# Kernel tuning notes

Measured on AMD Instinct MI355X. Metric: run time of the kernel, lower is better.

Reference implementation:

```python
import jax, jax.numpy as jnp
import numpy as np

B, N, C, H = 2, 2048, 1024, 16
D = C // H  # head dim
SCALE = D ** -0.5


def setup_inputs() -> dict:
    key = jax.random.key(0)
    k1, k2, k3 = jax.random.split(key, 3)
    x = jax.random.normal(k1, (B, N, C), dtype=jnp.float32)
    w_qkv = jax.random.normal(k2, (C, 3 * C), dtype=jnp.float32) * (C ** -0.5)
    w_proj = jax.random.normal(k3, (C, C), dtype=jnp.float32) * (C ** -0.5)
    b_proj = jnp.zeros((C,), dtype=jnp.float32)
    return {"x": x, "w_qkv": w_qkv, "w_proj": w_proj, "b_proj": b_proj}


def reference(x, w_qkv, w_proj, b_proj):
    # qkv projection: [B,N,3C] -> [3,B,H,N,D]
    qkv = (x @ w_qkv).reshape(B, N, 3, H, D).transpose(2, 0, 3, 1, 4)
    q, k, v = qkv[0], qkv[1], qkv[2]
    # attention scores [B,H,N,N]
    attn = jnp.einsum("bhnd,bhmd->bhnm", q, k) * SCALE
    attn = jax.nn.softmax(attn, axis=-1)
    # weighted values -> [B,N,C]
    out = jnp.einsum("bhnm,bhmd->bhnd", attn, v)
    out = out.transpose(0, 2, 1, 3).reshape(B, N, C)
    return out @ w_proj + b_proj
```

## Files before the change

kernel.cpp:

```cpp
#include <hip/hip_runtime.h>
#include <hip/hip_bf16.h>

#define BDIM 2
#define NSEQ 2048
#define CDIM 1024
#define HNUM 16
#define DDIM 64
#define QSCALE 0.18033688f

typedef __attribute__((ext_vector_type(4))) float f4;
typedef __attribute__((ext_vector_type(8))) short s8;

__device__ __forceinline__ unsigned short f2bf_hi(float f) {
  unsigned int u = __float_as_uint(f);
  u += 0x7fffu + ((u >> 16) & 1u);
  return (unsigned short)(u >> 16);
}
__device__ __forceinline__ unsigned int pack_bf16x2(float lo, float hi) {
  __hip_bfloat162 b2 = __float22bfloat162_rn(float2{lo, hi});
  union { __hip_bfloat162 b; unsigned int u; } c;
  c.b = b2;
  return c.u;
}
__device__ __forceinline__ float exp2_raw(float x) {
  float r;
  asm("v_exp_f32 %0, %1" : "=v"(r) : "v"(x));
  return r;
}
__device__ __forceinline__ void gll16(const void* g, void* l) {
  __builtin_amdgcn_global_load_lds(
      (const __attribute__((address_space(1))) unsigned int*)g,
      (__attribute__((address_space(3))) unsigned int*)l, 16, 0, 0);
}

__global__ __launch_bounds__(256)
void prep(const float* __restrict__ X, const float* __restrict__ Wq,
          const float* __restrict__ Wp,
          short* __restrict__ Xh, short* __restrict__ Wqh, short* __restrict__ Wph)
{
  __shared__ float T[64][65];
  const int bx = blockIdx.x;
  const int t = threadIdx.x;

  if (bx < 2048) {
    size_t i = ((size_t)bx * 256 + t) * 8;
    f4 a = *(const f4*)(X + i), b = *(const f4*)(X + i + 4);
    s8 h;
    #pragma unroll
    for (int j = 0; j < 4; ++j) h[j] = (short)f2bf_hi(a[j]);
    #pragma unroll
    for (int j = 0; j < 4; ++j) h[4 + j] = (short)f2bf_hi(b[j]);
    *(s8*)(Xh + i) = h;
    return;
  }

  const float* W;
  short* Th;
  int N, c0, k0;
  if (bx < 2816) {
    int b2 = bx - 2048;
    W = Wq; Th = Wqh; N = 3072;
    c0 = (b2 % 48) * 64; k0 = (b2 / 48) * 64;
  } else {
    int b2 = bx - 2816;
    W = Wp; Th = Wph; N = 1024;
    c0 = (b2 & 15) * 64; k0 = (b2 >> 4) * 64;
  }
  {
    const int r = t >> 2, c16 = (t & 3) * 16;
    const float* src = W + (size_t)(k0 + r) * N + c0 + c16;
    #pragma unroll
    for (int q = 0; q < 4; ++q) {
      f4 v = *(const f4*)(src + q * 4);
      #pragma unroll
      for (int j = 0; j < 4; ++j) T[c16 + q * 4 + j][r] = v[j];
    }
  }
  __syncthreads();
  {
    const int rr = t >> 2, k16 = (t & 3) * 16;
    s8 h0, h1;
    #pragma unroll
    for (int j = 0; j < 8; ++j) h0[j] = (short)f2bf_hi(T[rr][k16 + j]);
    #pragma unroll
    for (int j = 0; j < 8; ++j) h1[j] = (short)f2bf_hi(T[rr][k16 + 8 + j]);
    size_t o = (size_t)(c0 + rr) * 1024 + k0 + k16;
    *(s8*)(Th + o) = h0;
    *(s8*)(Th + o + 8) = h1;
  }
}

__global__ __launch_bounds__(256, 3)
void gemm_qkv(const short* __restrict__ Ah_g, const short* __restrict__ Bth,
              short* __restrict__ Qh, short* __restrict__ Kh, short* __restrict__ Vt)
{
  __shared__ __align__(16) short lds[2][2][128 * 32];
  const int t = threadIdx.x, w = t >> 6, lane = t & 63;
  const int fr = lane & 15, g = lane >> 4;
  const int wr = (w >> 1) * 64, wc = (w & 1) * 64;
  const int m0 = blockIdx.y * 128, c0 = blockIdx.x * 128;

  f4 acc[4][4];
  #pragma unroll
  for (int i = 0; i < 4; ++i)
    #pragma unroll
    for (int j = 0; j < 4; ++j)
      #pragma unroll
      for (int r = 0; r < 4; ++r) acc[i][j][r] = 0.f;

  auto stage = [&](int buf, int kt) {
    const int k0 = kt * 32;
    #pragma unroll
    for (int p = 0; p < 4; ++p) {
      const int plane = p >> 1;
      const int cid = (p & 1) * 256 + t;
      const int r = cid >> 2, c = cid & 3;
      const short* gsrc = (plane == 0)
          ? Ah_g + (size_t)(m0 + r) * 1024 + k0 + c * 8
          : Bth + (size_t)(c0 + r) * 1024 + k0 + c * 8;
      gll16(gsrc, &lds[buf][plane][(p & 1) * 2048 + w * 512]);
    }
  };

  auto compute = [&](int buf) {
    const short* A_h = lds[buf][0];
    const short* B_h = lds[buf][1];
    s8 ah[4], bh[4];
    #pragma unroll
    for (int i = 0; i < 4; ++i) ah[i] = *(const s8*)&A_h[(wr + i * 16 + fr) * 32 + g * 8];
    #pragma unroll
    for (int j = 0; j < 4; ++j) bh[j] = *(const s8*)&B_h[(wc + j * 16 + fr) * 32 + g * 8];
    #pragma unroll
    for (int i = 0; i < 4; ++i)
      #pragma unroll
      for (int j = 0; j < 4; ++j)
        acc[i][j] = __builtin_amdgcn_mfma_f32_16x16x32_bf16(ah[i], bh[j], acc[i][j], 0, 0, 0);
  };

  stage(0, 0);
  __syncthreads();
  int cur = 0;
  for (int kt = 0; kt < 32; ++kt) {
    if (kt + 1 < 32) stage(cur ^ 1, kt + 1);
    compute(cur);
    __syncthreads();
    cur ^= 1;
  }

  const int ts = c0 >> 10;
  const int rbase = g * 4;
  if (ts == 2) {
    #pragma unroll
    for (int i = 0; i < 4; ++i)
      #pragma unroll
      for (int j = 0; j < 4; ++j) {
        int grow = m0 + wr + i * 16 + rbase;
        int gcol = c0 + wc + j * 16 + fr;
        int b = grow >> 11, n = grow & 2047;
        int rem = gcol & 1023, hh = rem >> 6, d = rem & 63;
        short4 pv;
        pv.x = (short)f2bf_hi(acc[i][j][0]);
        pv.y = (short)f2bf_hi(acc[i][j][1]);
        pv.z = (short)f2bf_hi(acc[i][j][2]);
        pv.w = (short)f2bf_hi(acc[i][j][3]);
        *(short4*)(Vt + (((size_t)(b * 16 + hh)) * 64 + d) * 2048 + n) = pv;
      }
  } else {
    #pragma unroll
    for (int i = 0; i < 4; ++i)
      #pragma unroll
      for (int j = 0; j < 4; ++j)
        #pragma unroll
        for (int rr = 0; rr < 4; ++rr) {
          int grow = m0 + wr + i * 16 + rbase + rr;
          int gcol = c0 + wc + j * 16 + fr;
          int b = grow >> 11, n = grow & 2047;
          int rem = gcol & 1023, hh = rem >> 6, d = rem & 63;
          size_t o = (((size_t)(b * 16 + hh)) * 2048 + n) * 64 + d;
          float v = acc[i][j][rr];
          if (ts == 0) Qh[o] = (short)f2bf_hi(v * QSCALE);
          else         Kh[o] = (short)f2bf_hi(v);
        }
  }
}

__global__ __launch_bounds__(512, 2)
void attn(const short* __restrict__ Qh, const short* __restrict__ Kh,
          const short* __restrict__ Vt,
          short* __restrict__ AOh)
{
  __shared__ __align__(16) short kb[2][64 * 64], vb[2][64 * 64];
  __shared__ __align__(16) short pb[8][16][88];
  const int t = threadIdx.x, w = t >> 6, lane = t & 63;
  const int fr = lane & 15, g = lane >> 4;
  const int bid = blockIdx.x;
  const int swz = (bid & 7) * 64 + (bid >> 3);
  const int bh = swz >> 4, qb = swz & 15, q0 = qb * 128;
  const size_t base = (size_t)bh * 2048 * 64;

  s8 qf[2];
  {
    const int qrow = q0 + w * 16 + fr;
    #pragma unroll
    for (int ks = 0; ks < 2; ++ks)
      qf[ks] = *(const s8*)(Qh + base + (size_t)qrow * 64 + ks * 32 + g * 8);
  }

  s8 onesf;
  #pragma unroll
  for (int i = 0; i < 8; ++i) onesf[i] = (short)0x3F80;

  f4 oacc[4], lacc;
  #pragma unroll
  for (int dj = 0; dj < 4; ++dj)
    #pragma unroll
    for (int r = 0; r < 4; ++r) oacc[dj][r] = 0.f;
  #pragma unroll
  for (int r = 0; r < 4; ++r) lacc[r] = 0.f;

  auto stage = [&](int buf, int kt) {
    const int kv0 = kt * 64;
    const int r = t >> 3, csw = t & 7, cl = csw ^ (r & 7);
    gll16(Kh + base + (size_t)(kv0 + r) * 64 + cl * 8, &kb[buf][t * 8]);
    gll16(Vt + base + (size_t)r * 2048 + kv0 + cl * 8, &vb[buf][t * 8]);
  };

  auto body = [&](const short* kbuf, const short* vbuf) {
    f4 st[4];
    #pragma unroll
    for (int j = 0; j < 4; ++j)
      #pragma unroll
      for (int r = 0; r < 4; ++r) st[j][r] = 0.f;
    __builtin_amdgcn_s_setprio(1);
    #pragma unroll
    for (int j = 0; j < 4; ++j) {
      const int R = j * 16 + fr;
      #pragma unroll
      for (int ks = 0; ks < 2; ++ks) {
        const int co = ((ks * 4 + g) ^ (R & 7)) * 8;
        s8 khf = *(const s8*)&kbuf[R * 64 + co];
        st[j] = __builtin_amdgcn_mfma_f32_16x16x32_bf16(khf, qf[ks], st[j], 0, 0, 0);
      }
    }
    __builtin_amdgcn_s_setprio(0);

    #pragma unroll
    for (int j = 0; j < 4; ++j) {
      float p0 = exp2_raw(st[j][0]);
      float p1 = exp2_raw(st[j][1]);
      float p2 = exp2_raw(st[j][2]);
      float p3 = exp2_raw(st[j][3]);
      uint2 wv;
      wv.x = pack_bf16x2(p0, p1);
      wv.y = pack_bf16x2(p2, p3);
      *(uint2*)&pb[w][fr][j * 16 + g * 4] = wv;
    }

    __builtin_amdgcn_s_setprio(1);
    #pragma unroll
    for (int ks = 0; ks < 2; ++ks) {
      s8 paf = *(const s8*)&pb[w][fr][ks * 32 + g * 8];
      #pragma unroll
      for (int dj = 0; dj < 4; ++dj) {
        const int R = dj * 16 + fr;
        const int co = ((ks * 4 + g) ^ (R & 7)) * 8;
        s8 vbf = *(const s8*)&vbuf[R * 64 + co];
        oacc[dj] = __builtin_amdgcn_mfma_f32_16x16x32_bf16(paf, vbf, oacc[dj], 0, 0, 0);
      }
      lacc = __builtin_amdgcn_mfma_f32_16x16x32_bf16(paf, onesf, lacc, 0, 0, 0);
    }
    __builtin_amdgcn_s_setprio(0);
  };

  stage(0, 0);
  for (int kt = 0; kt < 32; kt += 2) {
    __syncthreads();
    stage(1, kt + 1);
    body(kb[0], vb[0]);
    __syncthreads();
    if (kt + 2 < 32) stage(0, kt + 2);
    body(kb[1], vb[1]);
  }

  const int b = bh >> 4, h = bh & 15;
  float linv[4];
  #pragma unroll
  for (int r = 0; r < 4; ++r) linv[r] = 1.f / lacc[r];
  #pragma unroll
  for (int dj = 0; dj < 4; ++dj)
    #pragma unroll
    for (int rr = 0; rr < 4; ++rr) {
      int n = q0 + w * 16 + g * 4 + rr;
      int col = h * 64 + dj * 16 + fr;
      size_t o = ((size_t)b * 2048 + n) * 1024 + col;
      AOh[o] = (short)f2bf_hi(oacc[dj][rr] * linv[rr]);
    }
}

__global__ __launch_bounds__(256, 2)
void gemm_proj(const short* __restrict__ Ah_g, const short* __restrict__ Bth,
               const float* __restrict__ bias, float* __restrict__ OUT)
{
  __shared__ __align__(16) short la[2][4096], lb[2][2048];
  const int t = threadIdx.x, w = t >> 6, lane = t & 63;
  const int fr = lane & 15, g = lane >> 4;
  const int wr = (w >> 1) * 64, wc = (w & 1) * 32;
  const int m0 = blockIdx.y * 128, c0 = blockIdx.x * 64;

  f4 acc[4][2];
  #pragma unroll
  for (int i = 0; i < 4; ++i)
    #pragma unroll
    for (int j = 0; j < 2; ++j)
      #pragma unroll
      for (int r = 0; r < 4; ++r) acc[i][j][r] = 0.f;

  auto stage = [&](int buf, int kt) {
    const int k0 = kt * 32;
    #pragma unroll
    for (int p = 0; p < 2; ++p) {
      const int cid = p * 256 + t;
      const int r = cid >> 2, c = cid & 3;
      gll16(Ah_g + (size_t)(m0 + r) * 1024 + k0 + c * 8, la[buf] + cid * 8);
    }
    {
      const int r = t >> 2, c = t & 3;
      gll16(Bth + (size_t)(c0 + r) * 1024 + k0 + c * 8, lb[buf] + t * 8);
    }
  };

  auto compute = [&](int buf) {
    s8 ah[4], bhf[2];
    #pragma unroll
    for (int i = 0; i < 4; ++i) ah[i] = *(const s8*)&la[buf][(wr + i * 16 + fr) * 32 + g * 8];
    #pragma unroll
    for (int j = 0; j < 2; ++j) bhf[j] = *(const s8*)&lb[buf][(wc + j * 16 + fr) * 32 + g * 8];
    #pragma unroll
    for (int i = 0; i < 4; ++i)
      #pragma unroll
      for (int j = 0; j < 2; ++j)
        acc[i][j] = __builtin_amdgcn_mfma_f32_16x16x32_bf16(ah[i], bhf[j], acc[i][j], 0, 0, 0);
  };

  stage(0, 0);
  __syncthreads();
  int cur = 0;
  for (int kt = 0; kt < 32; ++kt) {
    if (kt + 1 < 32) stage(cur ^ 1, kt + 1);
    compute(cur);
    __syncthreads();
    cur ^= 1;
  }

  const int rbase = g * 4;
  #pragma unroll
  for (int i = 0; i < 4; ++i)
    #pragma unroll
    for (int j = 0; j < 2; ++j)
      #pragma unroll
      for (int rr = 0; rr < 4; ++rr) {
        int grow = m0 + wr + i * 16 + rbase + rr;
        int gcol = c0 + wc + j * 16 + fr;
        OUT[(size_t)grow * 1024 + gcol] = acc[i][j][rr] + bias[gcol];
      }
}

extern "C" void kernel_launch(void* const* d_in, const int* in_sizes, int n_in,
                              void* d_out, int out_size, void* d_ws, size_t ws_size,
                              hipStream_t stream) {
  const float* x      = (const float*)d_in[0];
  const float* w_qkv  = (const float*)d_in[1];
  const float* w_proj = (const float*)d_in[2];
  const float* b_proj = (const float*)d_in[3];
  short* ws = (short*)d_ws;

  const size_t SW = (size_t)3072 * 1024;
  const size_t SP = (size_t)1024 * 1024;
  const size_t SX = (size_t)4096 * 1024;
  short* Wqh = ws;
  short* Wph = Wqh + SW;
  short* Xh  = Wph + SP;
  short* Qh  = Xh + SX;
  short* Kh  = Qh + SX;
  short* Vt  = Kh + SX;
  short* AOh = Xh;

  prep<<<3072, 256, 0, stream>>>(x, w_qkv, w_proj, Xh, Wqh, Wph);
  gemm_qkv<<<dim3(24, 32), 256, 0, stream>>>(Xh, Wqh, Qh, Kh, Vt);
  attn<<<512, 512, 0, stream>>>(Qh, Kh, Vt, AOh);
  gemm_proj<<<dim3(16, 32), 256, 0, stream>>>(AOh, Wph, b_proj, (float*)d_out);
}
```

Measured before the change: 117.4 us.

## Software-pipeline attention loop: overlap QK of tile k with PV of tile k-1

Restructures the attention inner loop so each phase issues the QK^T MFMAs for the current KV tile together with the PV MFMAs for the previous tile, whose probabilities are already in LDS. The exp and pack step then runs on the new scores. This is meant to hide the exp/LDS round-trip latency behind independent matrix work and give the scheduler more interleaving. In exchange it adds a prologue and an epilogue, keeps K and V of different tiles live in the double buffers, and changes the synchronisation pattern, which could add barrier stalls or register pressure.

```diff
diff --git a/kernel.cpp b/kernel.cpp
--- a/kernel.cpp
+++ b/kernel.cpp
@@ -225,12 +225,18 @@
     gll16(Vt + base + (size_t)r * 2048 + kv0 + cl * 8, &vb[buf][t * 8]);
   };
 
-  auto body = [&](const short* kbuf, const short* vbuf) {
+  auto phase = [&](const short* kbuf, const short* vbuf, int do_pv) {
+    s8 pa0, pa1;
+    if (do_pv) {
+      pa0 = *(const s8*)&pb[w][fr][0 * 32 + g * 8];
+      pa1 = *(const s8*)&pb[w][fr][1 * 32 + g * 8];
+    }
     f4 st[4];
     #pragma unroll
     for (int j = 0; j < 4; ++j)
       #pragma unroll
       for (int r = 0; r < 4; ++r) st[j][r] = 0.f;
+
     __builtin_amdgcn_s_setprio(1);
     #pragma unroll
     for (int j = 0; j < 4; ++j) {
@@ -241,6 +247,24 @@
         s8 khf = *(const s8*)&kbuf[R * 64 + co];
         st[j] = __builtin_amdgcn_mfma_f32_16x16x32_bf16(khf, qf[ks], st[j], 0, 0, 0);
       }
+    }
+    if (do_pv) {
+      #pragma unroll
+      for (int dj = 0; dj < 4; ++dj) {
+        const int R = dj * 16 + fr;
+        const int co0 = ((0 + g) ^ (R & 7)) * 8;
+        s8 vbf = *(const s8*)&vbuf[R * 64 + co0];
+        oacc[dj] = __builtin_amdgcn_mfma_f32_16x16x32_bf16(pa0, vbf, oacc[dj], 0, 0, 0);
+      }
+      lacc = __builtin_amdgcn_mfma_f32_16x16x32_bf16(pa0, onesf, lacc, 0, 0, 0);
+      #pragma unroll
+      for (int dj = 0; dj < 4; ++dj) {
+        const int R = dj * 16 + fr;
+        const int co1 = ((4 + g) ^ (R & 7)) * 8;
+        s8 vbf = *(const s8*)&vbuf[R * 64 + co1];
+        oacc[dj] = __builtin_amdgcn_mfma_f32_16x16x32_bf16(pa1, vbf, oacc[dj], 0, 0, 0);
+      }
+      lacc = __builtin_amdgcn_mfma_f32_16x16x32_bf16(pa1, onesf, lacc, 0, 0, 0);
     }
     __builtin_amdgcn_s_setprio(0);
 
@@ -255,31 +279,42 @@
       wv.y = pack_bf16x2(p2, p3);
       *(uint2*)&pb[w][fr][j * 16 + g * 4] = wv;
     }
-
+  };
+
+  stage(0, 0);
+  __syncthreads();
+  phase(kb[0], vb[0], 0);
+  __syncthreads();
+  stage(1, 1);
+  for (int kt = 1; kt < 32; ++kt) {
+    const int cur = kt & 1;
+    __syncthreads();
+    phase(kb[cur], vb[cur ^ 1], 1);
+    __syncthreads();
+    if (kt < 31) stage(cur ^ 1, kt + 1);
+  }
+  {
+    s8 pa0 = *(const s8*)&pb[w][fr][0 * 32 + g * 8];
+    s8 pa1 = *(const s8*)&pb[w][fr][1 * 32 + g * 8];
+    const short* vbuf = vb[1];
     __builtin_amdgcn_s_setprio(1);
     #pragma unroll
-    for (int ks = 0; ks < 2; ++ks) {
-      s8 paf = *(const s8*)&pb[w][fr][ks * 32 + g * 8];
-      #pragma unroll
-      for (int dj = 0; dj < 4; ++dj) {
-        const int R = dj * 16 + fr;
-        const int co = ((ks * 4 + g) ^ (R & 7)) * 8;
-        s8 vbf = *(const s8*)&vbuf[R * 64 + co];
-        oacc[dj] = __builtin_amdgcn_mfma_f32_16x16x32_bf16(paf, vbf, oacc[dj], 0, 0, 0);
-      }
-      lacc = __builtin_amdgcn_mfma_f32_16x16x32_bf16(paf, onesf, lacc, 0, 0, 0);
-    }
+    for (int dj = 0; dj < 4; ++dj) {
+      const int R = dj * 16 + fr;
+      const int co0 = ((0 + g) ^ (R & 7)) * 8;
+      s8 vbf = *(const s8*)&vbuf[R * 64 + co0];
+      oacc[dj] = __builtin_amdgcn_mfma_f32_16x16x32_bf16(pa0, vbf, oacc[dj], 0, 0, 0);
+    }
+    lacc = __builtin_amdgcn_mfma_f32_16x16x32_bf16(pa0, onesf, lacc, 0, 0, 0);
+    #pragma unroll
+    for (int dj = 0; dj < 4; ++dj) {
+      const int R = dj * 16 + fr;
+      const int co1 = ((4 + g) ^ (R & 7)) * 8;
+      s8 vbf = *(const s8*)&vbuf[R * 64 + co1];
+      oacc[dj] = __builtin_amdgcn_mfma_f32_16x16x32_bf16(pa1, vbf, oacc[dj], 0, 0, 0);
+    }
+    lacc = __builtin_amdgcn_mfma_f32_16x16x32_bf16(pa1, onesf, lacc, 0, 0, 0);
     __builtin_amdgcn_s_setprio(0);
-  };
-
-  stage(0, 0);
-  for (int kt = 0; kt < 32; kt += 2) {
-    __syncthreads();
-    stage(1, kt + 1);
-    body(kb[0], vb[0]);
-    __syncthreads();
-    if (kt + 2 < 32) stage(0, kt + 2);
-    body(kb[1], vb[1]);
   }
 
   const int b = bh >> 4, h = bh & 15;
```

Result: no change. 117.0 us (-0.4%).

## Process two query sub-tiles per wave in attention, halving block threads

Applied to the files above, without the earlier changes.

The attention kernel now runs 4 waves per block instead of 8, and each wave handles 32 query rows as two 16-row sub-tiles. Every K and V fragment read from LDS feeds two MFMAs, which halves LDS fragment traffic per unit of compute. In exchange each wave carries more accumulator and score registers, which may reduce occupancy, and each thread now issues twice as many staging loads.

```diff
diff --git a/kernel.cpp b/kernel.cpp
--- a/kernel.cpp
+++ b/kernel.cpp
@@ -184,13 +184,13 @@
   }
 }
 
-__global__ __launch_bounds__(512, 2)
+__global__ __launch_bounds__(256, 2)
 void attn(const short* __restrict__ Qh, const short* __restrict__ Kh,
           const short* __restrict__ Vt,
           short* __restrict__ AOh)
 {
   __shared__ __align__(16) short kb[2][64 * 64], vb[2][64 * 64];
-  __shared__ __align__(16) short pb[8][16][88];
+  __shared__ __align__(16) short pb[4][32][88];
   const int t = threadIdx.x, w = t >> 6, lane = t & 63;
   const int fr = lane & 15, g = lane >> 4;
   const int bid = blockIdx.x;
@@ -198,39 +198,49 @@
   const int bh = swz >> 4, qb = swz & 15, q0 = qb * 128;
   const size_t base = (size_t)bh * 2048 * 64;
 
-  s8 qf[2];
-  {
-    const int qrow = q0 + w * 16 + fr;
+  s8 qf[2][2];
+  #pragma unroll
+  for (int qs = 0; qs < 2; ++qs) {
+    const int qrow = q0 + w * 32 + qs * 16 + fr;
     #pragma unroll
     for (int ks = 0; ks < 2; ++ks)
-      qf[ks] = *(const s8*)(Qh + base + (size_t)qrow * 64 + ks * 32 + g * 8);
+      qf[qs][ks] = *(const s8*)(Qh + base + (size_t)qrow * 64 + ks * 32 + g * 8);
   }
 
   s8 onesf;
   #pragma unroll
   for (int i = 0; i < 8; ++i) onesf[i] = (short)0x3F80;
 
-  f4 oacc[4], lacc;
-  #pragma unroll
-  for (int dj = 0; dj < 4; ++dj)
-    #pragma unroll
-    for (int r = 0; r < 4; ++r) oacc[dj][r] = 0.f;
-  #pragma unroll
-  for (int r = 0; r < 4; ++r) lacc[r] = 0.f;
+  f4 oacc[2][4], lacc[2];
+  #pragma unroll
+  for (int qs = 0; qs < 2; ++qs) {
+    #pragma unroll
+    for (int dj = 0; dj < 4; ++dj)
+      #pragma unroll
+      for (int r = 0; r < 4; ++r) oacc[qs][dj][r] = 0.f;
+    #pragma unroll
+    for (int r = 0; r < 4; ++r) lacc[qs][r] = 0.f;
+  }
 
   auto stage = [&](int buf, int kt) {
     const int kv0 = kt * 64;
-    const int r = t >> 3, csw = t & 7, cl = csw ^ (r & 7);
-    gll16(Kh + base + (size_t)(kv0 + r) * 64 + cl * 8, &kb[buf][t * 8]);
-    gll16(Vt + base + (size_t)r * 2048 + kv0 + cl * 8, &vb[buf][t * 8]);
+    #pragma unroll
+    for (int p = 0; p < 2; ++p) {
+      const int cid = p * 256 + t;
+      const int r = cid >> 3, csw = cid & 7, cl = csw ^ (r & 7);
+      gll16(Kh + base + (size_t)(kv0 + r) * 64 + cl * 8, &kb[buf][cid * 8]);
+      gll16(Vt + base + (size_t)r * 2048 + kv0 + cl * 8, &vb[buf][cid * 8]);
+    }
   };
 
   auto body = [&](const short* kbuf, const short* vbuf) {
-    f4 st[4];
+    f4 st[4][2];
     #pragma unroll
     for (int j = 0; j < 4; ++j)
       #pragma unroll
-      for (int r = 0; r < 4; ++r) st[j][r] = 0.f;
+      for (int qs = 0; qs < 2; ++qs)
+        #pragma unroll
+        for (int r = 0; r < 4; ++r) st[j][qs][r] = 0.f;
     __builtin_amdgcn_s_setprio(1);
     #pragma unroll
     for (int j = 0; j < 4; ++j) {
@@ -239,35 +249,41 @@
       for (int ks = 0; ks < 2; ++ks) {
         const int co = ((ks * 4 + g) ^ (R & 7)) * 8;
         s8 khf = *(const s8*)&kbuf[R * 64 + co];
-        st[j] = __builtin_amdgcn_mfma_f32_16x16x32_bf16(khf, qf[ks], st[j], 0, 0, 0);
+        st[j][0] = __builtin_amdgcn_mfma_f32_16x16x32_bf16(khf, qf[0][ks], st[j][0], 0, 0, 0);
+        st[j][1] = __builtin_amdgcn_mfma_f32_16x16x32_bf16(khf, qf[1][ks], st[j][1], 0, 0, 0);
       }
     }
     __builtin_amdgcn_s_setprio(0);
 
     #pragma unroll
-    for (int j = 0; j < 4; ++j) {
-      float p0 = exp2_raw(st[j][0]);
-      float p1 = exp2_raw(st[j][1]);
-      float p2 = exp2_raw(st[j][2]);
-      float p3 = exp2_raw(st[j][3]);
-      uint2 wv;
-      wv.x = pack_bf16x2(p0, p1);
-      wv.y = pack_bf16x2(p2, p3);
-      *(uint2*)&pb[w][fr][j * 16 + g * 4] = wv;
-    }
+    for (int qs = 0; qs < 2; ++qs)
+      #pragma unroll
+      for (int j = 0; j < 4; ++j) {
+        float p0 = exp2_raw(st[j][qs][0]);
+        float p1 = exp2_raw(st[j][qs][1]);
+        float p2 = exp2_raw(st[j][qs][2]);
+        float p3 = exp2_raw(st[j][qs][3]);
+        uint2 wv;
+        wv.x = pack_bf16x2(p0, p1);
+        wv.y = pack_bf16x2(p2, p3);
+        *(uint2*)&pb[w][qs * 16 + fr][j * 16 + g * 4] = wv;
+      }
 
     __builtin_amdgcn_s_setprio(1);
     #pragma unroll
     for (int ks = 0; ks < 2; ++ks) {
-      s8 paf = *(const s8*)&pb[w][fr][ks * 32 + g * 8];
+      s8 pa0 = *(const s8*)&pb[w][0 * 16 + fr][ks * 32 + g * 8];
+      s8 pa1 = *(const s8*)&pb[w][1 * 16 + fr][ks * 32 + g * 8];
       #pragma unroll
       for (int dj = 0; dj < 4; ++dj) {
         const int R = dj * 16 + fr;
         const int co = ((ks * 4 + g) ^ (R & 7)) * 8;
         s8 vbf = *(const s8*)&vbuf[R * 64 + co];
-        oacc[dj] = __builtin_amdgcn_mfma_f32_16x16x32_bf16(paf, vbf, oacc[dj], 0, 0, 0);
-      }
-      lacc = __builtin_amdgcn_mfma_f32_16x16x32_bf16(paf, onesf, lacc, 0, 0, 0);
+        oacc[0][dj] = __builtin_amdgcn_mfma_f32_16x16x32_bf16(pa0, vbf, oacc[0][dj], 0, 0, 0);
+        oacc[1][dj] = __builtin_amdgcn_mfma_f32_16x16x32_bf16(pa1, vbf, oacc[1][dj], 0, 0, 0);
+      }
+      lacc[0] = __builtin_amdgcn_mfma_f32_16x16x32_bf16(pa0, onesf, lacc[0], 0, 0, 0);
+      lacc[1] = __builtin_amdgcn_mfma_f32_16x16x32_bf16(pa1, onesf, lacc[1], 0, 0, 0);
     }
     __builtin_amdgcn_s_setprio(0);
   };
@@ -283,18 +299,21 @@
   }
 
   const int b = bh >> 4, h = bh & 15;
-  float linv[4];
-  #pragma unroll
-  for (int r = 0; r < 4; ++r) linv[r] = 1.f / lacc[r];
-  #pragma unroll
-  for (int dj = 0; dj < 4; ++dj)
-    #pragma unroll
-    for (int rr = 0; rr < 4; ++rr) {
-      int n = q0 + w * 16 + g * 4 + rr;
-      int col = h * 64 + dj * 16 + fr;
-      size_t o = ((size_t)b * 2048 + n) * 1024 + col;
-      AOh[o] = (short)f2bf_hi(oacc[dj][rr] * linv[rr]);
-    }
+  #pragma unroll
+  for (int qs = 0; qs < 2; ++qs) {
+    float linv[4];
+    #pragma unroll
+    for (int r = 0; r < 4; ++r) linv[r] = 1.f / lacc[qs][r];
+    #pragma unroll
+    for (int dj = 0; dj < 4; ++dj)
+      #pragma unroll
+      for (int rr = 0; rr < 4; ++rr) {
+        int n = q0 + w * 32 + qs * 16 + g * 4 + rr;
+        int col = h * 64 + dj * 16 + fr;
+        size_t o = ((size_t)b * 2048 + n) * 1024 + col;
+        AOh[o] = (short)f2bf_hi(oacc[qs][dj][rr] * linv[rr]);
+      }
+  }
 }
 
 __global__ __launch_bounds__(256, 2)
@@ -387,6 +406,6 @@
 
   prep<<<3072, 256, 0, stream>>>(x, w_qkv, w_proj, Xh, Wqh, Wph);
   gemm_qkv<<<dim3(24, 32), 256, 0, stream>>>(Xh, Wqh, Qh, Kh, Vt);
-  attn<<<512, 512, 0, stream>>>(Qh, Kh, Vt, AOh);
+  attn<<<512, 256, 0, stream>>>(Qh, Kh, Vt, AOh);
   gemm_proj<<<dim3(16, 32), 256, 0, stream>>>(AOh, Wph, b_proj, (float*)d_out);
 }
```

Measured after the change: 118.8 us. About the same (+1.2%).

## Load attention K/V directly from global and deepen projection GEMM K-tile with swizzle

Applied to the files above, without the earlier changes.

The attention kernel drops its double-buffered LDS staging of K and V and reads MFMA operand fragments straight from global memory each iteration, which removes the block barriers and LDS traffic. The projection GEMM doubles its K-tile to 64 with an XOR-swizzled LDS layout, halving loop iterations and barriers, and raises the occupancy hint to 3 blocks. The attention change relies on caches to absorb the redundant per-wave global reads and exposes more load latency.

```diff
diff --git a/kernel.cpp b/kernel.cpp
--- a/kernel.cpp
+++ b/kernel.cpp
@@ -189,7 +189,6 @@
           const short* __restrict__ Vt,
           short* __restrict__ AOh)
 {
-  __shared__ __align__(16) short kb[2][64 * 64], vb[2][64 * 64];
   __shared__ __align__(16) short pb[8][16][88];
   const int t = threadIdx.x, w = t >> 6, lane = t & 63;
   const int fr = lane & 15, g = lane >> 4;
@@ -218,14 +217,9 @@
   #pragma unroll
   for (int r = 0; r < 4; ++r) lacc[r] = 0.f;
 
-  auto stage = [&](int buf, int kt) {
+  for (int kt = 0; kt < 32; ++kt) {
     const int kv0 = kt * 64;
-    const int r = t >> 3, csw = t & 7, cl = csw ^ (r & 7);
-    gll16(Kh + base + (size_t)(kv0 + r) * 64 + cl * 8, &kb[buf][t * 8]);
-    gll16(Vt + base + (size_t)r * 2048 + kv0 + cl * 8, &vb[buf][t * 8]);
-  };
-
-  auto body = [&](const short* kbuf, const short* vbuf) {
+
     f4 st[4];
     #pragma unroll
     for (int j = 0; j < 4; ++j)
@@ -237,8 +231,7 @@
       const int R = j * 16 + fr;
       #pragma unroll
       for (int ks = 0; ks < 2; ++ks) {
-        const int co = ((ks * 4 + g) ^ (R & 7)) * 8;
-        s8 khf = *(const s8*)&kbuf[R * 64 + co];
+        s8 khf = *(const s8*)(Kh + base + (size_t)(kv0 + R) * 64 + ks * 32 + g * 8);
         st[j] = __builtin_amdgcn_mfma_f32_16x16x32_bf16(khf, qf[ks], st[j], 0, 0, 0);
       }
     }
@@ -263,23 +256,12 @@
       #pragma unroll
       for (int dj = 0; dj < 4; ++dj) {
         const int R = dj * 16 + fr;
-        const int co = ((ks * 4 + g) ^ (R & 7)) * 8;
-        s8 vbf = *(const s8*)&vbuf[R * 64 + co];
+        s8 vbf = *(const s8*)(Vt + base + (size_t)R * 2048 + kv0 + ks * 32 + g * 8);
         oacc[dj] = __builtin_amdgcn_mfma_f32_16x16x32_bf16(paf, vbf, oacc[dj], 0, 0, 0);
       }
       lacc = __builtin_amdgcn_mfma_f32_16x16x32_bf16(paf, onesf, lacc, 0, 0, 0);
     }
     __builtin_amdgcn_s_setprio(0);
-  };
-
-  stage(0, 0);
-  for (int kt = 0; kt < 32; kt += 2) {
-    __syncthreads();
-    stage(1, kt + 1);
-    body(kb[0], vb[0]);
-    __syncthreads();
-    if (kt + 2 < 32) stage(0, kt + 2);
-    body(kb[1], vb[1]);
   }
 
   const int b = bh >> 4, h = bh & 15;
@@ -297,11 +279,11 @@
     }
 }
 
-__global__ __launch_bounds__(256, 2)
+__global__ __launch_bounds__(256, 3)
 void gemm_proj(const short* __restrict__ Ah_g, const short* __restrict__ Bth,
                const float* __restrict__ bias, float* __restrict__ OUT)
 {
-  __shared__ __align__(16) short la[2][4096], lb[2][2048];
+  __shared__ __align__(16) short la[2][128 * 64], lb[2][64 * 64];
   const int t = threadIdx.x, w = t >> 6, lane = t & 63;
   const int fr = lane & 15, g = lane >> 4;
   const int wr = (w >> 1) * 64, wc = (w & 1) * 32;
@@ -316,37 +298,50 @@
       for (int r = 0; r < 4; ++r) acc[i][j][r] = 0.f;
 
   auto stage = [&](int buf, int kt) {
-    const int k0 = kt * 32;
+    const int k0 = kt * 64;
+    #pragma unroll
+    for (int p = 0; p < 4; ++p) {
+      const int cid = p * 256 + t;
+      const int r = cid >> 3, csw = cid & 7, cl = csw ^ (r & 7);
+      gll16(Ah_g + (size_t)(m0 + r) * 1024 + k0 + cl * 8, la[buf] + cid * 8);
+    }
     #pragma unroll
     for (int p = 0; p < 2; ++p) {
       const int cid = p * 256 + t;
-      const int r = cid >> 2, c = cid & 3;
-      gll16(Ah_g + (size_t)(m0 + r) * 1024 + k0 + c * 8, la[buf] + cid * 8);
-    }
-    {
-      const int r = t >> 2, c = t & 3;
-      gll16(Bth + (size_t)(c0 + r) * 1024 + k0 + c * 8, lb[buf] + t * 8);
+      const int r = cid >> 3, csw = cid & 7, cl = csw ^ (r & 7);
+      gll16(Bth + (size_t)(c0 + r) * 1024 + k0 + cl * 8, lb[buf] + cid * 8);
     }
   };
 
   auto compute = [&](int buf) {
-    s8 ah[4], bhf[2];
-    #pragma unroll
-    for (int i = 0; i < 4; ++i) ah[i] = *(const s8*)&la[buf][(wr + i * 16 + fr) * 32 + g * 8];
-    #pragma unroll
-    for (int j = 0; j < 2; ++j) bhf[j] = *(const s8*)&lb[buf][(wc + j * 16 + fr) * 32 + g * 8];
-    #pragma unroll
-    for (int i = 0; i < 4; ++i)
-      #pragma unroll
-      for (int j = 0; j < 2; ++j)
-        acc[i][j] = __builtin_amdgcn_mfma_f32_16x16x32_bf16(ah[i], bhf[j], acc[i][j], 0, 0, 0);
+    #pragma unroll
+    for (int ks = 0; ks < 2; ++ks) {
+      s8 ah[4], bhf[2];
+      #pragma unroll
+      for (int i = 0; i < 4; ++i) {
+        const int R = wr + i * 16 + fr;
+        const int co = ((ks * 4 + g) ^ (R & 7)) * 8;
+        ah[i] = *(const s8*)&la[buf][R * 64 + co];
+      }
+      #pragma unroll
+      for (int j = 0; j < 2; ++j) {
+        const int R = wc + j * 16 + fr;
+        const int co = ((ks * 4 + g) ^ (R & 7)) * 8;
+        bhf[j] = *(const s8*)&lb[buf][R * 64 + co];
+      }
+      #pragma unroll
+      for (int i = 0; i < 4; ++i)
+        #pragma unroll
+        for (int j = 0; j < 2; ++j)
+          acc[i][j] = __builtin_amdgcn_mfma_f32_16x16x32_bf16(ah[i], bhf[j], acc[i][j], 0, 0, 0);
+    }
   };
 
   stage(0, 0);
   __syncthreads();
   int cur = 0;
-  for (int kt = 0; kt < 32; ++kt) {
-    if (kt + 1 < 32) stage(cur ^ 1, kt + 1);
+  for (int kt = 0; kt < 16; ++kt) {
+    if (kt + 1 < 16) stage(cur ^ 1, kt + 1);
     compute(cur);
     __syncthreads();
     cur ^= 1;
```

After: 288.9 us. +146.0%, slower.
